# Kernel tuning notes

Measured on AMD Instinct MI355X. Metric: run time of the kernel, lower is better.

Reference implementation:

```python
import jax, jax.numpy as jnp
import numpy as np

NUM_HEADS = 16
NEG_INF = -9e15


def setup_inputs() -> dict:
    key = jax.random.key(0)
    k1, k2, k3 = jax.random.split(key, 3)
    B, S, D = 2, 2048, 1024
    # xavier-uniform-ish init scale for weights
    lim_qkv = float(np.sqrt(6.0 / (D + 3 * D)))
    lim_o = float(np.sqrt(6.0 / (D + D)))
    return {
        "x": jax.random.normal(k1, (B, S, D), dtype=jnp.float32),
        "w_qkv": jax.random.uniform(k2, (3 * D, D), minval=-lim_qkv, maxval=lim_qkv, dtype=jnp.float32),
        "b_qkv": jnp.zeros((3 * D,), dtype=jnp.float32),
        "w_o": jax.random.uniform(k3, (D, D), minval=-lim_o, maxval=lim_o, dtype=jnp.float32),
        "b_o": jnp.zeros((D,), dtype=jnp.float32),
    }


def reference(x, w_qkv, b_qkv, w_o, b_o):
    B, S, D = x.shape
    H = NUM_HEADS
    hd = D // H
    # qkv projection: [B,S,3D]
    qkv = x @ w_qkv.T + b_qkv
    # -> [B, H, S, 3*hd], then split
    qkv = qkv.reshape(B, S, H, 3 * hd).transpose(0, 2, 1, 3)
    q, k, v = jnp.split(qkv, 3, axis=-1)  # each [B,H,S,hd]
    scale = 1.0 / jnp.sqrt(jnp.asarray(hd, dtype=x.dtype))
    logits = jnp.einsum("bhqd,bhkd->bhqk", q, k) * scale
    attn = jax.nn.softmax(logits, axis=-1)
    vals = jnp.einsum("bhqk,bhkd->bhqd", attn, v)
    vals = vals.transpose(0, 2, 1, 3).reshape(B, S, D)
    return vals @ w_o.T + b_o
```

## Files before the change

kernel.cpp:

```cpp
#include <hip/hip_runtime.h>
#include <math.h>

#define NHEADS 16
#define HD 64

typedef __attribute__((ext_vector_type(8))) _Float16 half8;
typedef __attribute__((ext_vector_type(4))) _Float16 half4;
typedef __attribute__((ext_vector_type(4))) float f32x4;
typedef __attribute__((ext_vector_type(16))) float f32x16;
typedef __attribute__((ext_vector_type(4))) unsigned int u32x4;

__device__ inline void load_lds16(const void* g, void* l) {
    __builtin_amdgcn_global_load_lds(
        (const __attribute__((address_space(1))) unsigned int*)g,
        (__attribute__((address_space(3))) unsigned int*)l, 16, 0, 0);
}
__device__ inline void pl32swap(unsigned int& x, unsigned int& y) {
    asm volatile("v_permlane32_swap_b32 %0, %1" : "+v"(x), "+v"(y));
}

#define NX  4194304
#define NWQ 3145728
#define NWO 1048576
__global__ void cvt_all(const float* __restrict__ x, const float* __restrict__ wq,
                        const float* __restrict__ wo, _Float16* __restrict__ xf,
                        _Float16* __restrict__ wqf, _Float16* __restrict__ wof) {
    int i = (blockIdx.x * blockDim.x + threadIdx.x) * 8;
    const float* src; _Float16* dst; int off;
    if (i < NX)            { src = x;  dst = xf;  off = i; }
    else if (i < NX + NWQ) { src = wq; dst = wqf; off = i - NX; }
    else                   { src = wo; dst = wof; off = i - (NX + NWQ); }
    float4 a = *(const float4*)(src + off);
    float4 b = *(const float4*)(src + off + 4);
    half8 h;
    h[0] = (_Float16)a.x; h[1] = (_Float16)a.y; h[2] = (_Float16)a.z; h[3] = (_Float16)a.w;
    h[4] = (_Float16)b.x; h[5] = (_Float16)b.y; h[6] = (_Float16)b.z; h[7] = (_Float16)b.w;
    *(half8*)(dst + off) = h;
}

#define GEMM_CORE(K)                                                                   \
    __shared__ __align__(1024) unsigned char smem[16384];                              \
    const int tid = threadIdx.x;                                                       \
    const int l = tid & 63, w = tid >> 6;                                              \
    const int wr = w >> 1, wc = w & 1;                                                 \
    const int nwg = gridDim.x * gridDim.y;                                             \
    const int bid = blockIdx.y * gridDim.x + blockIdx.x;                               \
    const int swz = (bid & 7) * (nwg >> 3) + (bid >> 3);                               \
    const int m0 = (swz / gridDim.x) * 128, n0 = (swz % gridDim.x) * 128;              \
    const int srow = tid >> 2;                                                         \
    const int schunk = (tid & 3) ^ ((srow >> 1) & 3);                                  \
    const size_t gA0 = (size_t)(m0 + srow) * K + schunk * 8;                           \
    const size_t gA1 = gA0 + (size_t)64 * K;                                           \
    const size_t gB0 = (size_t)(n0 + srow) * K + schunk * 8;                           \
    const size_t gB1 = gB0 + (size_t)64 * K;                                           \
    unsigned char* ldsW = smem + w * 1024;                                             \
    const int col16 = l & 15, kc = l >> 4;                                             \
    const int ra0 = wr * 64 + col16;                                                   \
    const int offA = ra0 * 64 + ((kc ^ ((ra0 >> 1) & 3)) * 16);                        \
    const int rb0 = wc * 64 + col16;                                                   \
    const int offB = rb0 * 64 + ((kc ^ ((rb0 >> 1) & 3)) * 16);                        \
    f32x4 acc[4][4] = {};                                                              \
    for (int k0 = 0; k0 < K; k0 += 32) {                                               \
        load_lds16(A + gA0 + k0, ldsW + 0);                                            \
        load_lds16(A + gA1 + k0, ldsW + 4096);                                         \
        load_lds16(B + gB0 + k0, ldsW + 8192);                                         \
        load_lds16(B + gB1 + k0, ldsW + 12288);                                       \
        __syncthreads();                                                               \
        half8 af[4], bf[4];                                                            \
        _Pragma("unroll")                                                              \
        for (int m = 0; m < 4; ++m) af[m] = *(const half8*)(smem + offA + m * 1024);   \
        _Pragma("unroll")                                                              \
        for (int n = 0; n < 4; ++n) bf[n] = *(const half8*)(smem + 8192 + offB + n * 1024); \
        _Pragma("unroll")                                                              \
        for (int m = 0; m < 4; ++m)                                                    \
            _Pragma("unroll")                                                          \
            for (int n = 0; n < 4; ++n)                                                \
                acc[m][n] = __builtin_amdgcn_mfma_f32_16x16x32_f16(af[m], bf[n], acc[m][n], 0, 0, 0); \
        __syncthreads();                                                               \
    }

__global__ __launch_bounds__(256, 2) void gemm_o(
    const _Float16* __restrict__ A, const _Float16* __restrict__ B,
    const float* __restrict__ bias, float* __restrict__ C,
    int M, int N, int K) {
    GEMM_CORE(K)
    const int rowb = m0 + wr * 64 + (l >> 4) * 4;
    const int colb = n0 + wc * 64 + col16;
    float bv[4];
    #pragma unroll
    for (int n = 0; n < 4; ++n) bv[n] = bias[colb + n * 16];
    #pragma unroll
    for (int m = 0; m < 4; ++m)
        #pragma unroll
        for (int j = 0; j < 4; ++j) {
            float* crow = C + (size_t)(rowb + m * 16 + j) * N + colb;
            #pragma unroll
            for (int n = 0; n < 4; ++n) crow[n * 16] = acc[m][n][j] + bv[n];
        }
}

#define QSCALE 0.18033688f
__global__ __launch_bounds__(256, 2) void gemm_qkv(
    const _Float16* __restrict__ A, const _Float16* __restrict__ B,
    const float* __restrict__ bias,
    _Float16* __restrict__ Qf, _Float16* __restrict__ Kf,
    _Float16* __restrict__ VfT, int K) {
    GEMM_CORE(K)
    const int rowb = m0 + wr * 64 + (l >> 4) * 4;
    const int colb = n0 + wc * 64 + col16;
    #pragma unroll
    for (int n = 0; n < 4; ++n) {
        int col = colb + n * 16;
        int h = col / 192;
        int rem = col - h * 192;
        int part = rem >> 6, d = rem & 63;
        float bv = bias[col];
        #pragma unroll
        for (int m = 0; m < 4; ++m) {
            int r0 = rowb + m * 16;
            int b = r0 >> 11, s0r = r0 & 2047;
            int bh = b * 16 + h;
            if (part == 0) {
                #pragma unroll
                for (int j = 0; j < 4; ++j)
                    Qf[((size_t)bh * 2048 + s0r + j) * 64 + d] =
                        (_Float16)((acc[m][n][j] + bv) * QSCALE);
            } else if (part == 1) {
                #pragma unroll
                for (int j = 0; j < 4; ++j)
                    Kf[((size_t)bh * 2048 + s0r + j) * 64 + d] = (_Float16)(acc[m][n][j] + bv);
            } else {
                half4 pk;
                pk[0] = (_Float16)(acc[m][n][0] + bv);
                pk[1] = (_Float16)(acc[m][n][1] + bv);
                pk[2] = (_Float16)(acc[m][n][2] + bv);
                pk[3] = (_Float16)(acc[m][n][3] + bv);
                *(half4*)&VfT[((size_t)bh * 64 + d) * 2048 + s0r] = pk;
            }
        }
    }
}

__global__ __launch_bounds__(512, 2) void mfma_attn(
    const _Float16* __restrict__ Qf, const _Float16* __restrict__ Kf,
    const _Float16* __restrict__ VfT, _Float16* __restrict__ vals) {
    __shared__ __align__(1024) unsigned char smem[40960];
    const int tid = threadIdx.x;
    const int l = tid & 63, w = tid >> 6;
    const int l31 = l & 31, hl = l >> 5;
    const int hwbid = blockIdx.y * gridDim.x + blockIdx.x;
    const int q_t = (hwbid >> 3) & 7;
    const int bh = (hwbid & 7) + ((hwbid >> 6) << 3);
    const int q0 = q_t * 256;
    const int h = bh & 15, b = bh >> 4;

    half8 qf[4];
    {
        const _Float16* qp = Qf + ((size_t)bh * 2048 + q0 + w * 32 + l31) * 64 + hl * 8;
        #pragma unroll
        for (int c = 0; c < 4; ++c) qf[c] = *(const half8*)(qp + c * 16);
    }
    f32x16 zvec = {};
    f32x16 o0 = {}, o1 = {};
    float mshift = 0.f, lsum = 0.f;

    const _Float16* Kg = Kf + (size_t)bh * 2048 * 64;
    const _Float16* Vg = VfT + (size_t)bh * 64 * 2048;

    int offK, offV;
    {
        int row2 = w * 4 + (l >> 4);
        int slot = (l & 15) ^ (row2 & 15);
        int row = row2 * 2 + (slot >> 3);
        int chunk = slot & 7;
        offK = row * 64 + chunk * 8;
        offV = row * 2048 + chunk * 8;
    }
    const int sbase = (l31 & 1) * 8;
    const int xr = (l31 >> 1) & 15;
    const int rb0 = (l31 >> 1) * 256;

    #define STAGE(kt0, kbuf, vbuf)                                                     \
        {                                                                              \
            unsigned char* bK = smem + (kbuf) * 8192 + w * 1024;                       \
            unsigned char* bV = smem + 16384 + (vbuf) * 8192 + w * 1024;               \
            load_lds16(Kg + (size_t)(kt0) * 64 + offK, bK);                            \
            load_lds16(Vg + (kt0) + offV, bV);                                         \
        }

    #define QK_TILE(kb, D0, D1)                                                        \
        {                                                                              \
            const unsigned char* Ksb_ = smem + (kb) * 8192;                            \
            __builtin_amdgcn_s_setprio(1);                                             \
            {                                                                          \
                int chOff = ((sbase + hl) ^ xr) << 4;                                  \
                half8 k0_ = *(const half8*)(Ksb_ + rb0 + chOff);                       \
                half8 k1_ = *(const half8*)(Ksb_ + rb0 + 4096 + chOff);                \
                D0 = __builtin_amdgcn_mfma_f32_32x32x16_f16(k0_, qf[0], zvec, 0, 0, 0);\
                D1 = __builtin_amdgcn_mfma_f32_32x32x16_f16(k1_, qf[0], zvec, 0, 0, 0);\
            }                                                                          \
            _Pragma("unroll")                                                          \
            for (int kc = 1; kc < 4; ++kc) {                                           \
                int chOff = ((sbase + kc * 2 + hl) ^ xr) << 4;                         \
                half8 k0_ = *(const half8*)(Ksb_ + rb0 + chOff);                       \
                half8 k1_ = *(const half8*)(Ksb_ + rb0 + 4096 + chOff);                \
                D0 = __builtin_amdgcn_mfma_f32_32x32x16_f16(k0_, qf[kc], D0, 0, 0, 0); \
                D1 = __builtin_amdgcn_mfma_f32_32x32x16_f16(k1_, qf[kc], D1, 0, 0, 0); \
            }                                                                          \
            __builtin_amdgcn_s_setprio(0);                                             \
        }

    #define SMPV(S0, S1)                                                               \
        {                                                                              \
            const unsigned char* Vsb_ = smem + 16384 + vrd * 8192;                     \
            if (__any(mshift != 0.f)) {                                                \
                _Pragma("unroll")                                                      \
                for (int r = 0; r < 16; ++r) { S0[r] -= mshift; S1[r] -= mshift; }     \
            }                                                                          \
            float r0 = 0.f, r1 = 0.f, r2 = 0.f, r3 = 0.f;                              \
            unsigned int a[2][8];                                                      \
            _Pragma("unroll")                                                          \
            for (int j = 0; j < 8; ++j) {                                              \
                float p0 = __builtin_amdgcn_exp2f(S0[2 * j]);                          \
                float p1 = __builtin_amdgcn_exp2f(S0[2 * j + 1]);                      \
                float q0_ = __builtin_amdgcn_exp2f(S1[2 * j]);                         \
                float q1_ = __builtin_amdgcn_exp2f(S1[2 * j + 1]);                     \
                r0 += p0; r1 += p1; r2 += q0_; r3 += q1_;                              \
                a[0][j] = __builtin_bit_cast(unsigned int, __builtin_amdgcn_cvt_pkrtz(p0, p1));   \
                a[1][j] = __builtin_bit_cast(unsigned int, __builtin_amdgcn_cvt_pkrtz(q0_, q1_)); \
            }                                                                          \
            float rsum = (r0 + r1) + (r2 + r3);                                        \
            if (__any(rsum > 32768.f)) {                                               \
                float pmax = S0[0];                                                    \
                _Pragma("unroll")                                                      \
                for (int r = 1; r < 16; ++r) pmax = fmaxf(pmax, S0[r]);                \
                _Pragma("unroll")                                                      \
                for (int r = 0; r < 16; ++r) pmax = fmaxf(pmax, S1[r]);                \
                pmax = fmaxf(pmax, __shfl_xor(pmax, 32, 64));                          \
                float d_ = fmaxf(pmax, 0.f);                                           \
                float corr = __builtin_amdgcn_exp2f(-d_);                              \
                _Pragma("unroll")                                                      \
                for (int r = 0; r < 16; ++r) { S0[r] -= d_; S1[r] -= d_; }             \
                _Pragma("unroll")                                                      \
                for (int r = 0; r < 16; ++r) { o0[r] *= corr; o1[r] *= corr; }         \
                lsum *= corr;                                                          \
                mshift += d_;                                                          \
                r0 = r1 = r2 = r3 = 0.f;                                               \
                _Pragma("unroll")                                                      \
                for (int j = 0; j < 8; ++j) {                                          \
                    float p0 = __builtin_amdgcn_exp2f(S0[2 * j]);                      \
                    float p1 = __builtin_amdgcn_exp2f(S0[2 * j + 1]);                  \
                    float q0_ = __builtin_amdgcn_exp2f(S1[2 * j]);                     \
                    float q1_ = __builtin_amdgcn_exp2f(S1[2 * j + 1]);                 \
                    r0 += p0; r1 += p1; r2 += q0_; r3 += q1_;                          \
                    a[0][j] = __builtin_bit_cast(unsigned int, __builtin_amdgcn_cvt_pkrtz(p0, p1));   \
                    a[1][j] = __builtin_bit_cast(unsigned int, __builtin_amdgcn_cvt_pkrtz(q0_, q1_)); \
                }                                                                      \
                rsum = (r0 + r1) + (r2 + r3);                                          \
            }                                                                          \
            lsum += rsum;                                                              \
            _Pragma("unroll")                                                          \
            for (int c = 0; c < 2; ++c) {                                              \
                pl32swap(a[c][0], a[c][2]);                                            \
                pl32swap(a[c][1], a[c][3]);                                            \
                pl32swap(a[c][4], a[c][6]);                                            \
                pl32swap(a[c][5], a[c][7]);                                            \
            }                                                                          \
            __builtin_amdgcn_s_setprio(1);                                             \
            _Pragma("unroll")                                                          \
            for (int kk = 0; kk < 4; ++kk) {                                           \
                u32x4 pw;                                                              \
                pw.x = a[kk >> 1][(kk & 1) * 4 + 0];                                   \
                pw.y = a[kk >> 1][(kk & 1) * 4 + 1];                                   \
                pw.z = a[kk >> 1][(kk & 1) * 4 + 2];                                   \
                pw.w = a[kk >> 1][(kk & 1) * 4 + 3];                                   \
                half8 pf = __builtin_bit_cast(half8, pw);                              \
                int chOff = ((sbase + kk * 2 + hl) ^ xr) << 4;                         \
                half8 v0 = *(const half8*)(Vsb_ + rb0 + chOff);                        \
                half8 v1 = *(const half8*)(Vsb_ + rb0 + 4096 + chOff);                 \
                o0 = __builtin_amdgcn_mfma_f32_32x32x16_f16(v0, pf, o0, 0, 0, 0);      \
                o1 = __builtin_amdgcn_mfma_f32_32x32x16_f16(v1, pf, o1, 0, 0, 0);      \
            }                                                                          \
            __builtin_amdgcn_s_setprio(0);                                             \
        }

    #define ITER(tt, kb, D0, D1, P0, P1, dostage)                                      \
        __syncthreads();                                                               \
        if (dostage) STAGE(((tt) + 1) * 64, (kb) ^ 1, vst)                             \
        QK_TILE(kb, D0, D1)                                                            \
        SMPV(P0, P1)                                                                   \
        vrd = (vrd == 2) ? 0 : vrd + 1;                                                \
        vst = (vst == 2) ? 0 : vst + 1;

    int vrd = 0, vst = 2;
    f32x16 sA0, sA1, sB0, sB1;

    STAGE(0, 0, 0)
    __syncthreads();
    QK_TILE(0, sA0, sA1)
    STAGE(64, 1, 1)

    for (int t = 1; t < 31; t += 2) {
        ITER(t, 1, sB0, sB1, sA0, sA1, 1)
        ITER(t + 1, 0, sA0, sA1, sB0, sB1, 1)
    }
    ITER(31, 1, sB0, sB1, sA0, sA1, 0)
    SMPV(sB0, sB1)

    lsum += __shfl_xor(lsum, 32, 64);
    float inv = 1.f / lsum;
    size_t orow = ((size_t)(b * 2048 + q0 + w * 32 + l31)) * 1024 + h * 64;
    #pragma unroll
    for (int dc = 0; dc < 2; ++dc) {
        const f32x16* op = dc ? &o1 : &o0;
        #pragma unroll
        for (int rq = 0; rq < 4; ++rq) {
            int d0 = dc * 32 + rq * 8 + hl * 4;
            half4 hv;
            #pragma unroll
            for (int j = 0; j < 4; ++j) hv[j] = (_Float16)((*op)[rq * 4 + j] * inv);
            *(half4*)(vals + orow + d0) = hv;
        }
    }
}

extern "C" void kernel_launch(void* const* d_in, const int* in_sizes, int n_in,
                              void* d_out, int out_size, void* d_ws, size_t ws_size,
                              hipStream_t stream) {
    const float* x     = (const float*)d_in[0];
    const float* w_qkv = (const float*)d_in[1];
    const float* b_qkv = (const float*)d_in[2];
    const float* w_o   = (const float*)d_in[3];
    const float* b_o   = (const float*)d_in[4];
    float* out = (float*)d_out;

    const int B = 2, S = 2048, D = 1024;
    const int M = B * S;
    const int N1 = 3 * D;
    const int BH = B * NHEADS;

    _Float16* xf  = (_Float16*)d_ws;
    _Float16* wqf = xf  + (size_t)M * D;
    _Float16* wof = wqf + (size_t)N1 * D;
    _Float16* Qf  = wof + (size_t)D * D;
    _Float16* Kf  = Qf  + (size_t)BH * S * HD;
    _Float16* VfT = Kf  + (size_t)BH * S * HD;
    _Float16* vals = xf;

    cvt_all<<<(NX + NWQ + NWO) / 2048, 256, 0, stream>>>(x, w_qkv, w_o, xf, wqf, wof);

    gemm_qkv<<<dim3(N1 / 128, M / 128), 256, 0, stream>>>(xf, wqf, b_qkv, Qf, Kf, VfT, D);

    mfma_attn<<<dim3(S / 256, BH), 512, 0, stream>>>(Qf, Kf, VfT, vals);

    gemm_o<<<dim3(D / 128, M / 128), 256, 0, stream>>>(vals, wof, b_o, out, M, D, D);
}
```

Before: 112.9 us.

## Shrink output-projection GEMM tile to 128x64 and drop attention setprio hints

The output projection GEMM gets its own 128x64 tile, with each wave covering 64x32 and a smaller LDS footprint, replacing the shared 128x128 core. The grid doubles to 512 workgroups, which spreads work across more CUs for the 4096x1024 output. Separately, the s_setprio raise/lower around the MFMA blocks in the attention kernel is removed. The smaller tile lowers data reuse per workgroup and raises redundant global loads of A, and dropping the priority hints may change how the attention kernel's waves interleave.

```diff
diff --git a/kernel.cpp b/kernel.cpp
--- a/kernel.cpp
+++ b/kernel.cpp
@@ -83,19 +83,55 @@
     const _Float16* __restrict__ A, const _Float16* __restrict__ B,
     const float* __restrict__ bias, float* __restrict__ C,
     int M, int N, int K) {
-    GEMM_CORE(K)
+    __shared__ __align__(1024) unsigned char smem[12288];
+    const int tid = threadIdx.x;
+    const int l = tid & 63, w = tid >> 6;
+    const int wr = w >> 1, wc = w & 1;
+    const int nwg = gridDim.x * gridDim.y;
+    const int bid = blockIdx.y * gridDim.x + blockIdx.x;
+    const int swz = (bid & 7) * (nwg >> 3) + (bid >> 3);
+    const int m0 = (swz / gridDim.x) * 128, n0 = (swz % gridDim.x) * 64;
+    const int srow = tid >> 2;
+    const int schunk = (tid & 3) ^ ((srow >> 1) & 3);
+    const size_t gA0 = (size_t)(m0 + srow) * K + schunk * 8;
+    const size_t gA1 = gA0 + (size_t)64 * K;
+    const size_t gB0 = (size_t)(n0 + srow) * K + schunk * 8;
+    unsigned char* ldsW = smem + w * 1024;
+    const int col16 = l & 15, kc = l >> 4;
+    const int ra0 = wr * 64 + col16;
+    const int offA = ra0 * 64 + ((kc ^ ((ra0 >> 1) & 3)) * 16);
+    const int rb0 = wc * 32 + col16;
+    const int offB = 8192 + rb0 * 64 + ((kc ^ ((rb0 >> 1) & 3)) * 16);
+    f32x4 acc[4][2] = {};
+    for (int k0 = 0; k0 < K; k0 += 32) {
+        load_lds16(A + gA0 + k0, ldsW + 0);
+        load_lds16(A + gA1 + k0, ldsW + 4096);
+        load_lds16(B + gB0 + k0, ldsW + 8192);
+        __syncthreads();
+        half8 af[4], bf[2];
+        #pragma unroll
+        for (int m = 0; m < 4; ++m) af[m] = *(const half8*)(smem + offA + m * 1024);
+        #pragma unroll
+        for (int n = 0; n < 2; ++n) bf[n] = *(const half8*)(smem + offB + n * 1024);
+        #pragma unroll
+        for (int m = 0; m < 4; ++m)
+            #pragma unroll
+            for (int n = 0; n < 2; ++n)
+                acc[m][n] = __builtin_amdgcn_mfma_f32_16x16x32_f16(af[m], bf[n], acc[m][n], 0, 0, 0);
+        __syncthreads();
+    }
     const int rowb = m0 + wr * 64 + (l >> 4) * 4;
-    const int colb = n0 + wc * 64 + col16;
-    float bv[4];
+    const int colb = n0 + wc * 32 + col16;
+    float bv[2];
     #pragma unroll
-    for (int n = 0; n < 4; ++n) bv[n] = bias[colb + n * 16];
+    for (int n = 0; n < 2; ++n) bv[n] = bias[colb + n * 16];
     #pragma unroll
     for (int m = 0; m < 4; ++m)
         #pragma unroll
         for (int j = 0; j < 4; ++j) {
             float* crow = C + (size_t)(rowb + m * 16 + j) * N + colb;
             #pragma unroll
-            for (int n = 0; n < 4; ++n) crow[n * 16] = acc[m][n][j] + bv[n];
+            for (int n = 0; n < 2; ++n) crow[n * 16] = acc[m][n][j] + bv[n];
         }
 }
 
@@ -191,7 +227,6 @@
     #define QK_TILE(kb, D0, D1)                                                        \
         {                                                                              \
             const unsigned char* Ksb_ = smem + (kb) * 8192;                            \
-            __builtin_amdgcn_s_setprio(1);                                             \
             {                                                                          \
                 int chOff = ((sbase + hl) ^ xr) << 4;                                  \
                 half8 k0_ = *(const half8*)(Ksb_ + rb0 + chOff);                       \
@@ -207,7 +242,6 @@
                 D0 = __builtin_amdgcn_mfma_f32_32x32x16_f16(k0_, qf[kc], D0, 0, 0, 0); \
                 D1 = __builtin_amdgcn_mfma_f32_32x32x16_f16(k1_, qf[kc], D1, 0, 0, 0); \
             }                                                                          \
-            __builtin_amdgcn_s_setprio(0);                                             \
         }
 
     #define SMPV(S0, S1)                                                               \
@@ -266,7 +300,6 @@
                 pl32swap(a[c][4], a[c][6]);                                            \
                 pl32swap(a[c][5], a[c][7]);                                            \
             }                                                                          \
-            __builtin_amdgcn_s_setprio(1);                                             \
             _Pragma("unroll")                                                          \
             for (int kk = 0; kk < 4; ++kk) {                                           \
                 u32x4 pw;                                                              \
@@ -281,7 +314,6 @@
                 o0 = __builtin_amdgcn_mfma_f32_32x32x16_f16(v0, pf, o0, 0, 0, 0);      \
                 o1 = __builtin_amdgcn_mfma_f32_32x32x16_f16(v1, pf, o1, 0, 0, 0);      \
             }                                                                          \
-            __builtin_amdgcn_s_setprio(0);                                             \
         }
 
     #define ITER(tt, kb, D0, D1, P0, P1, dostage)                                      \
@@ -353,5 +385,5 @@
 
     mfma_attn<<<dim3(S / 256, BH), 512, 0, stream>>>(Qf, Kf, VfT, vals);
 
-    gemm_o<<<dim3(D / 128, M / 128), 256, 0, stream>>>(vals, wof, b_o, out, M, D, D);
-}
+    gemm_o<<<dim3(D / 64, M / 128), 256, 0, stream>>>(vals, wof, b_o, out, M, D, D);
+}
```

After: 109.5 us. 1.03x faster.

## Triple-buffer GEMM and attention LDS loads with vmcnt-based waits, narrower gemm_o tiles

Applied to the files above, without the earlier changes.

Both GEMMs now use a three-stage LDS ring, issuing async global-to-LDS loads two steps ahead. Each step waits with an explicit s_waitcnt vmcnt and a single barrier, replacing the two __syncthreads per K step. The attention kernel moves from a software-pipelined QK/PV schedule with separate K and V buffers to a unified three-buffer ring, and drops the setprio hints. gemm_o switches to 128x64 tiles so it launches more workgroups. The goal is to hide global load latency and cut barrier stalls, at the cost of more LDS per block (which may reduce occupancy) and the loss of the previous QK/softmax overlap in attention.

```diff
diff --git a/kernel.cpp b/kernel.cpp
--- a/kernel.cpp
+++ b/kernel.cpp
@@ -38,66 +38,23 @@
     *(half8*)(dst + off) = h;
 }
 
-#define GEMM_CORE(K)                                                                   \
-    __shared__ __align__(1024) unsigned char smem[16384];                              \
+#define GEMM_SETUP(K, NTILE)                                                           \
     const int tid = threadIdx.x;                                                       \
     const int l = tid & 63, w = tid >> 6;                                              \
     const int wr = w >> 1, wc = w & 1;                                                 \
     const int nwg = gridDim.x * gridDim.y;                                             \
     const int bid = blockIdx.y * gridDim.x + blockIdx.x;                               \
     const int swz = (bid & 7) * (nwg >> 3) + (bid >> 3);                               \
-    const int m0 = (swz / gridDim.x) * 128, n0 = (swz % gridDim.x) * 128;              \
+    const int m0 = (swz / gridDim.x) * 128, n0 = (swz % gridDim.x) * (NTILE);          \
     const int srow = tid >> 2;                                                         \
     const int schunk = (tid & 3) ^ ((srow >> 1) & 3);                                  \
     const size_t gA0 = (size_t)(m0 + srow) * K + schunk * 8;                           \
     const size_t gA1 = gA0 + (size_t)64 * K;                                           \
     const size_t gB0 = (size_t)(n0 + srow) * K + schunk * 8;                           \
-    const size_t gB1 = gB0 + (size_t)64 * K;                                           \
     unsigned char* ldsW = smem + w * 1024;                                             \
     const int col16 = l & 15, kc = l >> 4;                                             \
     const int ra0 = wr * 64 + col16;                                                   \
-    const int offA = ra0 * 64 + ((kc ^ ((ra0 >> 1) & 3)) * 16);                        \
-    const int rb0 = wc * 64 + col16;                                                   \
-    const int offB = rb0 * 64 + ((kc ^ ((rb0 >> 1) & 3)) * 16);                        \
-    f32x4 acc[4][4] = {};                                                              \
-    for (int k0 = 0; k0 < K; k0 += 32) {                                               \
-        load_lds16(A + gA0 + k0, ldsW + 0);                                            \
-        load_lds16(A + gA1 + k0, ldsW + 4096);                                         \
-        load_lds16(B + gB0 + k0, ldsW + 8192);                                         \
-        load_lds16(B + gB1 + k0, ldsW + 12288);                                       \
-        __syncthreads();                                                               \
-        half8 af[4], bf[4];                                                            \
-        _Pragma("unroll")                                                              \
-        for (int m = 0; m < 4; ++m) af[m] = *(const half8*)(smem + offA + m * 1024);   \
-        _Pragma("unroll")                                                              \
-        for (int n = 0; n < 4; ++n) bf[n] = *(const half8*)(smem + 8192 + offB + n * 1024); \
-        _Pragma("unroll")                                                              \
-        for (int m = 0; m < 4; ++m)                                                    \
-            _Pragma("unroll")                                                          \
-            for (int n = 0; n < 4; ++n)                                                \
-                acc[m][n] = __builtin_amdgcn_mfma_f32_16x16x32_f16(af[m], bf[n], acc[m][n], 0, 0, 0); \
-        __syncthreads();                                                               \
-    }
-
-__global__ __launch_bounds__(256, 2) void gemm_o(
-    const _Float16* __restrict__ A, const _Float16* __restrict__ B,
-    const float* __restrict__ bias, float* __restrict__ C,
-    int M, int N, int K) {
-    GEMM_CORE(K)
-    const int rowb = m0 + wr * 64 + (l >> 4) * 4;
-    const int colb = n0 + wc * 64 + col16;
-    float bv[4];
-    #pragma unroll
-    for (int n = 0; n < 4; ++n) bv[n] = bias[colb + n * 16];
-    #pragma unroll
-    for (int m = 0; m < 4; ++m)
-        #pragma unroll
-        for (int j = 0; j < 4; ++j) {
-            float* crow = C + (size_t)(rowb + m * 16 + j) * N + colb;
-            #pragma unroll
-            for (int n = 0; n < 4; ++n) crow[n * 16] = acc[m][n][j] + bv[n];
-        }
-}
+    const int offA = ra0 * 64 + ((kc ^ ((ra0 >> 1) & 3)) * 16);
 
 #define QSCALE 0.18033688f
 __global__ __launch_bounds__(256, 2) void gemm_qkv(
@@ -105,7 +62,49 @@
     const float* __restrict__ bias,
     _Float16* __restrict__ Qf, _Float16* __restrict__ Kf,
     _Float16* __restrict__ VfT, int K) {
-    GEMM_CORE(K)
+    __shared__ __align__(1024) unsigned char smem[49152];
+    GEMM_SETUP(K, 128)
+    const size_t gB1 = gB0 + (size_t)64 * K;
+    const int rb0 = wc * 64 + col16;
+    const int offB = rb0 * 64 + ((kc ^ ((rb0 >> 1) & 3)) * 16);
+    f32x4 acc[4][4] = {};
+
+#define GSTAGE(k0_, buf_)                                                              \
+    load_lds16(A + gA0 + (k0_), ldsW + (buf_) * 16384 + 0);                            \
+    load_lds16(A + gA1 + (k0_), ldsW + (buf_) * 16384 + 4096);                         \
+    load_lds16(B + gB0 + (k0_), ldsW + (buf_) * 16384 + 8192);                         \
+    load_lds16(B + gB1 + (k0_), ldsW + (buf_) * 16384 + 12288);
+#define GSTEP(s_, buf_, VM, dostage)                                                   \
+    asm volatile("s_waitcnt " VM ::: "memory");                                        \
+    __builtin_amdgcn_sched_barrier(0);                                                 \
+    __builtin_amdgcn_s_barrier();                                                      \
+    if (dostage) { GSTAGE(((s_) + 2) * 32, ((buf_) + 2) % 3) }                         \
+    {                                                                                  \
+        const unsigned char* bs = smem + (buf_) * 16384;                               \
+        half8 af[4], bf[4];                                                            \
+        _Pragma("unroll")                                                              \
+        for (int m = 0; m < 4; ++m) af[m] = *(const half8*)(bs + offA + m * 1024);     \
+        _Pragma("unroll")                                                              \
+        for (int n = 0; n < 4; ++n) bf[n] = *(const half8*)(bs + 8192 + offB + n * 1024); \
+        _Pragma("unroll")                                                              \
+        for (int m = 0; m < 4; ++m)                                                    \
+            _Pragma("unroll")                                                          \
+            for (int n = 0; n < 4; ++n)                                                \
+                acc[m][n] = __builtin_amdgcn_mfma_f32_16x16x32_f16(af[m], bf[n], acc[m][n], 0, 0, 0); \
+    }
+
+    GSTAGE(0, 0)
+    GSTAGE(32, 1)
+    for (int t = 0; t < 30; t += 3) {
+        GSTEP(t, 0, "vmcnt(4)", 1)
+        GSTEP(t + 1, 1, "vmcnt(4)", 1)
+        GSTEP(t + 2, 2, "vmcnt(4)", 1)
+    }
+    GSTEP(30, 0, "vmcnt(4)", 0)
+    GSTEP(31, 1, "vmcnt(0)", 0)
+#undef GSTAGE
+#undef GSTEP
+
     const int rowb = m0 + wr * 64 + (l >> 4) * 4;
     const int colb = n0 + wc * 64 + col16;
     #pragma unroll
@@ -141,10 +140,70 @@
     }
 }
 
+__global__ __launch_bounds__(256, 2) void gemm_o(
+    const _Float16* __restrict__ A, const _Float16* __restrict__ B,
+    const float* __restrict__ bias, float* __restrict__ C,
+    int M, int N, int K) {
+    __shared__ __align__(1024) unsigned char smem[36864];
+    GEMM_SETUP(K, 64)
+    const int rb0 = wc * 32 + col16;
+    const int offB = rb0 * 64 + ((kc ^ ((rb0 >> 1) & 3)) * 16);
+    f32x4 acc[4][2] = {};
+
+#define OSTAGE(k0_, buf_)                                                              \
+    load_lds16(A + gA0 + (k0_), ldsW + (buf_) * 12288 + 0);                            \
+    load_lds16(A + gA1 + (k0_), ldsW + (buf_) * 12288 + 4096);                         \
+    load_lds16(B + gB0 + (k0_), ldsW + (buf_) * 12288 + 8192);
+#define OSTEP(s_, buf_, VM, dostage)                                                   \
+    asm volatile("s_waitcnt " VM ::: "memory");                                        \
+    __builtin_amdgcn_sched_barrier(0);                                                 \
+    __builtin_amdgcn_s_barrier();                                                      \
+    if (dostage) { OSTAGE(((s_) + 2) * 32, ((buf_) + 2) % 3) }                         \
+    {                                                                                  \
+        const unsigned char* bs = smem + (buf_) * 12288;                               \
+        half8 af[4], bf[2];                                                            \
+        _Pragma("unroll")                                                              \
+        for (int m = 0; m < 4; ++m) af[m] = *(const half8*)(bs + offA + m * 1024);     \
+        _Pragma("unroll")                                                              \
+        for (int n = 0; n < 2; ++n) bf[n] = *(const half8*)(bs + 8192 + offB + n * 1024); \
+        _Pragma("unroll")                                                              \
+        for (int m = 0; m < 4; ++m)                                                    \
+            _Pragma("unroll")                                                          \
+            for (int n = 0; n < 2; ++n)                                                \
+                acc[m][n] = __builtin_amdgcn_mfma_f32_16x16x32_f16(af[m], bf[n], acc[m][n], 0, 0, 0); \
+    }
+
+    OSTAGE(0, 0)
+    OSTAGE(32, 1)
+    for (int t = 0; t < 30; t += 3) {
+        OSTEP(t, 0, "vmcnt(3)", 1)
+        OSTEP(t + 1, 1, "vmcnt(3)", 1)
+        OSTEP(t + 2, 2, "vmcnt(3)", 1)
+    }
+    OSTEP(30, 0, "vmcnt(3)", 0)
+    OSTEP(31, 1, "vmcnt(0)", 0)
+#undef OSTAGE
+#undef OSTEP
+
+    const int rowb = m0 + wr * 64 + (l >> 4) * 4;
+    const int colb = n0 + wc * 32 + col16;
+    float bv[2];
+    #pragma unroll
+    for (int n = 0; n < 2; ++n) bv[n] = bias[colb + n * 16];
+    #pragma unroll
+    for (int m = 0; m < 4; ++m)
+        #pragma unroll
+        for (int j = 0; j < 4; ++j) {
+            float* crow = C + (size_t)(rowb + m * 16 + j) * N + colb;
+            #pragma unroll
+            for (int n = 0; n < 2; ++n) crow[n * 16] = acc[m][n][j] + bv[n];
+        }
+}
+
 __global__ __launch_bounds__(512, 2) void mfma_attn(
     const _Float16* __restrict__ Qf, const _Float16* __restrict__ Kf,
     const _Float16* __restrict__ VfT, _Float16* __restrict__ vals) {
-    __shared__ __align__(1024) unsigned char smem[40960];
+    __shared__ __align__(1024) unsigned char smem[49152];
     const int tid = threadIdx.x;
     const int l = tid & 63, w = tid >> 6;
     const int l31 = l & 31, hl = l >> 5;
@@ -180,10 +239,10 @@
     const int xr = (l31 >> 1) & 15;
     const int rb0 = (l31 >> 1) * 256;
 
-    #define STAGE(kt0, kbuf, vbuf)                                                     \
+    #define STAGE(kt0, buf)                                                            \
         {                                                                              \
-            unsigned char* bK = smem + (kbuf) * 8192 + w * 1024;                       \
-            unsigned char* bV = smem + 16384 + (vbuf) * 8192 + w * 1024;               \
+            unsigned char* bK = smem + (buf) * 8192 + w * 1024;                        \
+            unsigned char* bV = smem + 24576 + (buf) * 8192 + w * 1024;                \
             load_lds16(Kg + (size_t)(kt0) * 64 + offK, bK);                            \
             load_lds16(Vg + (kt0) + offV, bV);                                         \
         }
@@ -191,7 +250,6 @@
     #define QK_TILE(kb, D0, D1)                                                        \
         {                                                                              \
             const unsigned char* Ksb_ = smem + (kb) * 8192;                            \
-            __builtin_amdgcn_s_setprio(1);                                             \
             {                                                                          \
                 int chOff = ((sbase + hl) ^ xr) << 4;                                  \
                 half8 k0_ = *(const half8*)(Ksb_ + rb0 + chOff);                       \
@@ -207,12 +265,11 @@
                 D0 = __builtin_amdgcn_mfma_f32_32x32x16_f16(k0_, qf[kc], D0, 0, 0, 0); \
                 D1 = __builtin_amdgcn_mfma_f32_32x32x16_f16(k1_, qf[kc], D1, 0, 0, 0); \
             }                                                                          \
-            __builtin_amdgcn_s_setprio(0);                                             \
-        }
-
-    #define SMPV(S0, S1)                                                               \
+        }
+
+    #define SMPV(S0, S1, vb_)                                                          \
         {                                                                              \
-            const unsigned char* Vsb_ = smem + 16384 + vrd * 8192;                     \
+            const unsigned char* Vsb_ = smem + 24576 + (vb_) * 8192;                   \
             if (__any(mshift != 0.f)) {                                                \
                 _Pragma("unroll")                                                      \
                 for (int r = 0; r < 16; ++r) { S0[r] -= mshift; S1[r] -= mshift; }     \
@@ -266,7 +323,6 @@
                 pl32swap(a[c][4], a[c][6]);                                            \
                 pl32swap(a[c][5], a[c][7]);                                            \
             }                                                                          \
-            __builtin_amdgcn_s_setprio(1);                                             \
             _Pragma("unroll")                                                          \
             for (int kk = 0; kk < 4; ++kk) {                                           \
                 u32x4 pw;                                                              \
@@ -281,31 +337,26 @@
                 o0 = __builtin_amdgcn_mfma_f32_32x32x16_f16(v0, pf, o0, 0, 0, 0);      \
                 o1 = __builtin_amdgcn_mfma_f32_32x32x16_f16(v1, pf, o1, 0, 0, 0);      \
             }                                                                          \
-            __builtin_amdgcn_s_setprio(0);                                             \
-        }
-
-    #define ITER(tt, kb, D0, D1, P0, P1, dostage)                                      \
-        __syncthreads();                                                               \
-        if (dostage) STAGE(((tt) + 1) * 64, (kb) ^ 1, vst)                             \
-        QK_TILE(kb, D0, D1)                                                            \
-        SMPV(P0, P1)                                                                   \
-        vrd = (vrd == 2) ? 0 : vrd + 1;                                                \
-        vst = (vst == 2) ? 0 : vst + 1;
-
-    int vrd = 0, vst = 2;
-    f32x16 sA0, sA1, sB0, sB1;
-
-    STAGE(0, 0, 0)
-    __syncthreads();
-    QK_TILE(0, sA0, sA1)
-    STAGE(64, 1, 1)
-
-    for (int t = 1; t < 31; t += 2) {
-        ITER(t, 1, sB0, sB1, sA0, sA1, 1)
-        ITER(t + 1, 0, sA0, sA1, sB0, sB1, 1)
-    }
-    ITER(31, 1, sB0, sB1, sA0, sA1, 0)
-    SMPV(sB0, sB1)
+        }
+
+    #define AITER(tt, kb, VM, dostage)                                                 \
+        asm volatile("s_waitcnt " VM ::: "memory");                                    \
+        __builtin_amdgcn_sched_barrier(0);                                             \
+        __builtin_amdgcn_s_barrier();                                                  \
+        if (dostage) STAGE(((tt) + 2) * 64, ((kb) + 2) % 3)                            \
+        QK_TILE(kb, sS0, sS1)                                                          \
+        SMPV(sS0, sS1, kb)
+
+    STAGE(0, 0)
+    STAGE(64, 1)
+    f32x16 sS0, sS1;
+    for (int t = 0; t < 30; t += 3) {
+        AITER(t, 0, "vmcnt(2)", 1)
+        AITER(t + 1, 1, "vmcnt(2)", 1)
+        AITER(t + 2, 2, "vmcnt(2)", 1)
+    }
+    AITER(30, 0, "vmcnt(2)", 0)
+    AITER(31, 1, "vmcnt(0)", 0)
 
     lsum += __shfl_xor(lsum, 32, 64);
     float inv = 1.f / lsum;
@@ -353,5 +404,5 @@
 
     mfma_attn<<<dim3(S / 256, BH), 512, 0, stream>>>(Qf, Kf, VfT, vals);
 
-    gemm_o<<<dim3(D / 128, M / 128), 256, 0, stream>>>(vals, wof, b_o, out, M, D, D);
-}
+    gemm_o<<<dim3(D / 64, M / 128), 256, 0, stream>>>(vals, wof, b_o, out, M, D, D);
+}
```

Measured after the change: 107.2 us. 5.0% less time.
